# Performance work log

Hardware: AMD Instinct MI355X
Metric: run time of the kernel (lower is better)

## Reference

```python
import jax, jax.numpy as jnp
import numpy as np

B, N, D = 4, 2048, 1024
H = 16
HD = D // H          # 64
SCALE = 1.0 / HD     # module uses 1/head_dim (NOT 1/sqrt)
NEG = -10000.0       # masked_fill value used by the module
THETA = 10000.0


def setup_inputs() -> dict:
    key = jax.random.key(0)
    ks = jax.random.split(key, 6)
    s = (1.0 / D) ** 0.5  # init_method_normal((1/dim)**0.5)
    return {
        "x": jax.random.normal(ks[0], (B, N, D), jnp.float32),
        "Wq": jax.random.normal(ks[1], (D, D), jnp.float32) * s,
        "Wk": jax.random.normal(ks[2], (D, D), jnp.float32) * s,
        "Wv": jax.random.normal(ks[3], (D, D), jnp.float32) * s,
        "Wo": jax.random.normal(ks[4], (D, D), jnp.float32) * s,
        "bo": jnp.zeros((D,), jnp.float32),
    }


def _rope(t):
    # t: [b, h, n, d]; interleaved-pair rotary (lucidrains rotate_queries_or_keys)
    d, n = t.shape[-1], t.shape[-2]
    inv_freq = 1.0 / (THETA ** (jnp.arange(0, d, 2, dtype=jnp.float32) / d))  # [d/2]
    ang = jnp.arange(n, dtype=jnp.float32)[:, None] * inv_freq[None, :]        # [n, d/2]
    cos = jnp.repeat(jnp.cos(ang), 2, axis=-1)  # [n, d]
    sin = jnp.repeat(jnp.sin(ang), 2, axis=-1)
    x1, x2 = t[..., ::2], t[..., 1::2]
    rot = jnp.stack([-x2, x1], axis=-1).reshape(t.shape)  # rotate_half
    return t * cos + rot * sin


def reference(x, Wq, Wk, Wv, Wo, bo):
    b, n, _ = x.shape
    # QKV projections (no bias; torch Linear: x @ W.T)
    q = (x @ Wq.T).reshape(b, n, H, HD).transpose(0, 2, 1, 3)  # [b,h,n,d]
    k = (x @ Wk.T).reshape(b, n, H, HD).transpose(0, 2, 1, 3)
    v = (x @ Wv.T).reshape(b, n, H, HD).transpose(0, 2, 1, 3)
    # RoPE on q, k
    q = _rope(q)
    k = _rope(k)
    # additive mask: 0 on/below diagonal, -10000 above (causal_mask=True path)
    i = jnp.arange(n)
    add_mask = jnp.where(i[:, None] >= i[None, :], 0.0, NEG).astype(x.dtype)  # [n,n]
    scores = jnp.einsum("bhqd,bhkd->bhqk", q, k) * SCALE + add_mask
    attn = jax.nn.softmax(scores, axis=-1)
    out = jnp.einsum("bhqk,bhkd->bhqd", attn, v)            # [b,h,n,d]
    out = out.transpose(0, 2, 1, 3).reshape(b, n, H * HD)    # [b,n,D]
    return out @ Wo.T + bo
```

## Files before the change

### kernel.cpp

```cpp
#include <hip/hip_runtime.h>
#include <hip/hip_bf16.h>
#include <math.h>

#define B_ 4
#define N_ 2048
#define D_ 1024
#define H_ 16
#define HD_ 64
#define SCALE_ 0.015625f
#define MD_ ((size_t)B_ * N_ * D_)
#define DD_ ((size_t)D_ * D_)
#define BHSZ_ ((size_t)N_ * HD_)
#define QSC_ 0.0225421143f

typedef __hip_bfloat16 bf16;
typedef __attribute__((ext_vector_type(8))) __bf16 bf16x8;
typedef __attribute__((ext_vector_type(4))) float f32x4;
typedef __attribute__((ext_vector_type(16))) float f32x16;

__device__ __forceinline__ float b2f(bf16 x) { return __bfloat162float(x); }
__device__ __forceinline__ bf16 f2b(float x) { return __float2bfloat16(x); }

__device__ __forceinline__ unsigned int pk2(float a, float b) {
  union { bf16 h[2]; unsigned int u; } t;
  t.h[0] = f2b(a); t.h[1] = f2b(b);
  return t.u;
}
__device__ __forceinline__ unsigned int pk2t(float a, float b) {
  return (__float_as_uint(a) >> 16) | (__float_as_uint(b) & 0xffff0000u);
}

__device__ __forceinline__ void gl_lds16(const bf16* g, bf16* l) {
  __builtin_amdgcn_global_load_lds(
      (const __attribute__((address_space(1))) void*)g,
      (__attribute__((address_space(3))) void*)l, 16, 0, 0);
}

__global__ __launch_bounds__(256) void cvt_all(
    const float* __restrict__ x,  const float* __restrict__ wq,
    const float* __restrict__ wk, const float* __restrict__ wv,
    const float* __restrict__ wo, bf16* __restrict__ xb,
    bf16* __restrict__ wb)
{
  const int blk = blockIdx.x;
  const float* s; bf16* d; int i;
  if (blk < 4096)      { s = x;  d = xb;           i = blk; }
  else if (blk < 4608) { s = wq; d = wb;           i = blk - 4096; }
  else if (blk < 5120) { s = wk; d = wb + DD_;     i = blk - 4608; }
  else if (blk < 5632) { s = wv; d = wb + 2 * DD_; i = blk - 5120; }
  else                 { s = wo; d = wb + 3 * DD_; i = blk - 5632; }
  int e = (i * 256 + threadIdx.x) * 8;
  float4 a = *reinterpret_cast<const float4*>(s + e);
  float4 b = *reinterpret_cast<const float4*>(s + e + 4);
  bf16 t[8] = {f2b(a.x), f2b(a.y), f2b(a.z), f2b(a.w),
               f2b(b.x), f2b(b.y), f2b(b.z), f2b(b.w)};
  *reinterpret_cast<int4*>(d + e) = *reinterpret_cast<const int4*>(t);
}

template <int MODE>
__global__ __launch_bounds__(256) void mgemm(
    const bf16* __restrict__ A, const bf16* __restrict__ W,
    const float* __restrict__ bias, void* __restrict__ Cv,
    int M, int N, int K)
{
  __shared__ bf16 As[128 * 32];
  __shared__ bf16 Ws[128 * 32];

  const int tid  = threadIdx.x;
  const int w    = tid >> 6;
  const int lane = tid & 63;
  const int bm   = blockIdx.y * 128;
  const int bn   = blockIdx.x * 128;

  const int wr = (w >> 1) * 64;
  const int wc = (w & 1) * 64;
  const int lm   = lane & 15;
  const int quad = lane >> 4;

  const int srow = lane >> 2;
  const int sslot = (lane & 3) ^ ((lane >> 3) & 3);
  const int scol = sslot * 8;

  const int rsw  = (quad ^ ((lm >> 1) & 3)) * 8;

  f32x4 acc[4][4] = {};

  for (int k0 = 0; k0 < K; k0 += 32) {
#pragma unroll
    for (int cc = 0; cc < 2; ++cc) {
      int c = w * 2 + cc;
      int r = c * 16 + srow;
      gl_lds16(A + (size_t)(bm + r) * K + k0 + scol, &As[c * 512]);
      gl_lds16(W + (size_t)(bn + r) * K + k0 + scol, &Ws[c * 512]);
    }
    __syncthreads();

    bf16x8 af[4], bf_[4];
#pragma unroll
    for (int mi = 0; mi < 4; ++mi)
      af[mi] = *reinterpret_cast<const bf16x8*>(&As[(wr + mi * 16 + lm) * 32 + rsw]);
#pragma unroll
    for (int ni = 0; ni < 4; ++ni)
      bf_[ni] = *reinterpret_cast<const bf16x8*>(&Ws[(wc + ni * 16 + lm) * 32 + rsw]);

#pragma unroll
    for (int mi = 0; mi < 4; ++mi)
#pragma unroll
      for (int ni = 0; ni < 4; ++ni)
        acc[mi][ni] = __builtin_amdgcn_mfma_f32_16x16x32_bf16(
            af[mi], bf_[ni], acc[mi][ni], 0, 0, 0);
    __syncthreads();
  }

#pragma unroll
  for (int mi = 0; mi < 4; ++mi) {
#pragma unroll
    for (int r = 0; r < 4; ++r) {
      int row = bm + wr + mi * 16 + quad * 4 + r;
#pragma unroll
      for (int ni = 0; ni < 4; ++ni) {
        int col = bn + wc + ni * 16 + lm;
        float v = acc[mi][ni][r];
        if (MODE == 1) {
          v += bias[col];
          reinterpret_cast<float*>(Cv)[(size_t)row * N + col] = v;
        } else {
          int reg = col >> 10;
          int cc  = col & 1023;
          int bb  = row >> 11;
          int n   = row & (N_ - 1);
          int hh  = cc >> 6;
          int dd  = cc & 63;
          if (reg < 2) {
            int t32 = n >> 5, m = n & 31;
            int s = dd >> 4, hb = (dd >> 3) & 1, j = dd & 7;
            reinterpret_cast<bf16*>(Cv)[(size_t)reg * MD_ +
                (size_t)(bb * H_ + hh) * BHSZ_ +
                (size_t)t32 * 2048 + s * 512 + hb * 256 + m * 8 + j] = f2b(v);
          } else {
            int t32 = n >> 5, kk = n & 31;
            int hf = kk >> 4, hb = (kk >> 3) & 1, j = kk & 7;
            reinterpret_cast<bf16*>(Cv)[2 * MD_ +
                (size_t)(bb * H_ + hh) * BHSZ_ +
                (size_t)t32 * 2048 + hf * 1024 + hb * 512 + dd * 8 + j] = f2b(v);
          }
        }
      }
    }
  }
}

__global__ __launch_bounds__(256) void rope_inplace(bf16* __restrict__ qf,
                                                    bf16* __restrict__ kf)
{
  const int half = blockIdx.x >> 12;
  const int blk  = blockIdx.x & 4095;
  bf16* base = half ? kf : qf;
  const float LN_THETA = 9.210340371976184f;

  size_t e = ((size_t)blk * 256 + threadIdx.x) * 8;
  int within = (int)(e & (BHSZ_ - 1));
  int t32 = within >> 11;
  int rem = within & 2047;
  int s  = rem >> 9;
  int hb = (rem >> 8) & 1;
  int m  = (rem >> 3) & 31;
  int n  = t32 * 32 + m;

  uint4 raw = *reinterpret_cast<const uint4*>(base + e);
  unsigned int pr[4] = {raw.x, raw.y, raw.z, raw.w};
  unsigned int outw[4];
#pragma unroll
  for (int p = 0; p < 4; ++p) {
    int i = s * 8 + hb * 4 + p;
    float inv = __expf(-((float)(2 * i) / (float)HD_) * LN_THETA);
    float ang = (float)n * inv;
    float sv, cv;
    sincosf(ang, &sv, &cv);
    float a = b2f(((bf16*)&pr[p])[0]);
    float c = b2f(((bf16*)&pr[p])[1]);
    float r0 = a * cv - c * sv;
    float r1 = c * cv + a * sv;
    if (half == 0) { r0 *= QSC_; r1 *= QSC_; }
    outw[p] = pk2(r0, r1);
  }
  uint4 o = {outw[0], outw[1], outw[2], outw[3]};
  *reinterpret_cast<uint4*>(base + e) = o;
}

__global__ __launch_bounds__(128) void fattn4_kernel(
    const bf16* __restrict__ Qf, const bf16* __restrict__ Kf,
    const bf16* __restrict__ Vf, bf16* __restrict__ O)
{
  __shared__ float Ls[32 * 64];
  __shared__ float Ll[64];

  const int wv   = threadIdx.x >> 6;
  const int lane = threadIdx.x & 63;
  const int blk  = blockIdx.x;
  const int xcd  = blk & 7;
  const int j    = blk >> 3;
  const int qt   = 63 - (j >> 3);
  const int bh   = xcd * 8 + (j & 7);
  const int b    = bh >> 4;
  const int h    = bh & 15;
  const int col  = lane & 31;
  const int hi   = lane >> 5;

  const bf16* Qb = Qf + (size_t)bh * BHSZ_ + (size_t)qt * 2048 + hi * 256 + col * 8;
  const bf16* Kb = Kf + (size_t)bh * BHSZ_ + hi * 256 + col * 8;
  const bf16* Vb = Vf + (size_t)bh * BHSZ_ + hi * 512 + col * 8;

  bf16x8 qb[4];
#pragma unroll
  for (int s = 0; s < 4; ++s)
    qb[s] = *reinterpret_cast<const bf16x8*>(Qb + s * 512);

  f32x16 o0 = {}, o1 = {};
  float lsum = 0.f;

  for (int kst = wv; kst <= qt; kst += 2) {
    const bf16* kp = Kb + (size_t)kst * 2048;
    f32x16 st = {};
#pragma unroll
    for (int s = 0; s < 4; ++s) {
      bf16x8 ka = *reinterpret_cast<const bf16x8*>(kp + s * 512);
      st = __builtin_amdgcn_mfma_f32_32x32x16_bf16(ka, qb[s], st, 0, 0, 0);
    }

    float pe[16];
    if (kst == qt) {
#pragma unroll
      for (int r = 0; r < 16; ++r) {
        int koff = (r & 3) + 8 * (r >> 2) + 4 * hi;
        float e = (koff <= col) ? exp2f(st[r]) : 0.f;
        pe[r] = e; lsum += e;
      }
    } else {
#pragma unroll
      for (int r = 0; r < 16; ++r) {
        float e = exp2f(st[r]);
        pe[r] = e; lsum += e;
      }
    }

    const bf16* vp = Vb + (size_t)kst * 2048;
#pragma unroll
    for (int hf = 0; hf < 2; ++hf) {
      unsigned int a0 = pk2t(pe[8 * hf + 0], pe[8 * hf + 1]);
      unsigned int a1 = pk2t(pe[8 * hf + 2], pe[8 * hf + 3]);
      unsigned int b0 = pk2t(pe[8 * hf + 4], pe[8 * hf + 5]);
      unsigned int b1 = pk2t(pe[8 * hf + 6], pe[8 * hf + 7]);
      unsigned int s0 = hi ? a0 : b0;
      unsigned int s1 = hi ? a1 : b1;
      unsigned int r0 = (unsigned int)__shfl_xor((int)s0, 32);
      unsigned int r1 = (unsigned int)__shfl_xor((int)s1, 32);
      union { uint4 u; bf16x8 v; } pb;
      pb.u.x = hi ? r0 : a0;
      pb.u.y = hi ? r1 : a1;
      pb.u.z = hi ? b0 : r0;
      pb.u.w = hi ? b1 : r1;

      bf16x8 v0 = *reinterpret_cast<const bf16x8*>(vp + hf * 1024);
      bf16x8 v1 = *reinterpret_cast<const bf16x8*>(vp + hf * 1024 + 256);
      o0 = __builtin_amdgcn_mfma_f32_32x32x16_bf16(v0, pb.v, o0, 0, 0, 0);
      o1 = __builtin_amdgcn_mfma_f32_32x32x16_bf16(v1, pb.v, o1, 0, 0, 0);
    }
  }

  if (wv == 1) {
#pragma unroll
    for (int r = 0; r < 16; ++r) {
      Ls[r * 64 + lane]        = o0[r];
      Ls[(16 + r) * 64 + lane] = o1[r];
    }
    Ll[lane] = lsum;
  }
  __syncthreads();
  if (wv == 0) {
    float lt = lsum + Ll[lane];
    lt += __shfl_xor(lt, 32);
    float inv = 1.f / lt;
#pragma unroll
    for (int r = 0; r < 16; ++r) {
      o0[r] = (o0[r] + Ls[r * 64 + lane]) * inv;
      o1[r] = (o1[r] + Ls[(16 + r) * 64 + lane]) * inv;
    }
    bf16* Op = O + ((size_t)(b * N_ + 32 * qt + col)) * D_ + h * HD_;
#pragma unroll
    for (int g = 0; g < 4; ++g) {
      uint2 u;
      u.x = pk2(o0[4 * g + 0], o0[4 * g + 1]);
      u.y = pk2(o0[4 * g + 2], o0[4 * g + 3]);
      *reinterpret_cast<uint2*>(Op + 8 * g + 4 * hi) = u;
      u.x = pk2(o1[4 * g + 0], o1[4 * g + 1]);
      u.y = pk2(o1[4 * g + 2], o1[4 * g + 3]);
      *reinterpret_cast<uint2*>(Op + 32 + 8 * g + 4 * hi) = u;
    }
  }
}

extern "C" void kernel_launch(void* const* d_in, const int* in_sizes, int n_in,
                              void* d_out, int out_size, void* d_ws, size_t ws_size,
                              hipStream_t stream)
{
  const float* x  = (const float*)d_in[0];
  const float* Wq = (const float*)d_in[1];
  const float* Wk = (const float*)d_in[2];
  const float* Wv = (const float*)d_in[3];
  const float* Wo = (const float*)d_in[4];
  const float* bo = (const float*)d_in[5];
  float* out = (float*)d_out;

  const int M = B_ * N_;

  bf16* xb  = (bf16*)d_ws;
  bf16* qf  = xb + MD_;
  bf16* kf  = qf + MD_;
  bf16* vf  = kf + MD_;
  bf16* Wqb = vf + MD_;
  bf16* Wob = Wqb + 3 * DD_;
  bf16* ao  = xb;

  cvt_all<<<6144, 256, 0, stream>>>(x, Wq, Wk, Wv, Wo, xb, Wqb);

  mgemm<0><<<dim3(24, 64), 256, 0, stream>>>(xb, Wqb, nullptr, qf, M, 3 * D_, D_);

  rope_inplace<<<8192, 256, 0, stream>>>(qf, kf);

  fattn4_kernel<<<4096, 128, 0, stream>>>(qf, kf, vf, ao);

  mgemm<1><<<dim3(8, 64), 256, 0, stream>>>(ao, Wob, bo, out, M, D_, D_);
}
```

Before: 274.3 us.

## Give each attention wave its own query tile instead of splitting keys across waves

```diff
diff --git a/kernel.cpp b/kernel.cpp
--- a/kernel.cpp
+++ b/kernel.cpp
@@ -188,22 +188,20 @@
   *reinterpret_cast<uint4*>(base + e) = o;
 }
 
-__global__ __launch_bounds__(128) void fattn4_kernel(
+__global__ __launch_bounds__(128) void fattn5_kernel(
     const bf16* __restrict__ Qf, const bf16* __restrict__ Kf,
     const bf16* __restrict__ Vf, bf16* __restrict__ O)
 {
-  __shared__ float Ls[32 * 64];
-  __shared__ float Ll[64];
-
   const int wv   = threadIdx.x >> 6;
   const int lane = threadIdx.x & 63;
   const int blk  = blockIdx.x;
   const int xcd  = blk & 7;
-  const int j    = blk >> 3;
-  const int qt   = 63 - (j >> 3);
-  const int bh   = xcd * 8 + (j & 7);
+  const int jj   = blk >> 3;
+  const int j    = 31 - (jj >> 3);
+  const int bh   = xcd * 8 + (jj & 7);
   const int b    = bh >> 4;
   const int h    = bh & 15;
+  const int qt   = 2 * j + wv;
   const int col  = lane & 31;
   const int hi   = lane >> 5;
 
@@ -219,7 +217,7 @@
   f32x16 o0 = {}, o1 = {};
   float lsum = 0.f;
 
-  for (int kst = wv; kst <= qt; kst += 2) {
+  for (int kst = 0; kst <= qt; ++kst) {
     const bf16* kp = Kb + (size_t)kst * 2048;
     f32x16 st = {};
 #pragma unroll
@@ -268,35 +266,21 @@
     }
   }
 
-  if (wv == 1) {
-#pragma unroll
-    for (int r = 0; r < 16; ++r) {
-      Ls[r * 64 + lane]        = o0[r];
-      Ls[(16 + r) * 64 + lane] = o1[r];
-    }
-    Ll[lane] = lsum;
-  }
-  __syncthreads();
-  if (wv == 0) {
-    float lt = lsum + Ll[lane];
-    lt += __shfl_xor(lt, 32);
-    float inv = 1.f / lt;
-#pragma unroll
-    for (int r = 0; r < 16; ++r) {
-      o0[r] = (o0[r] + Ls[r * 64 + lane]) * inv;
-      o1[r] = (o1[r] + Ls[(16 + r) * 64 + lane]) * inv;
-    }
-    bf16* Op = O + ((size_t)(b * N_ + 32 * qt + col)) * D_ + h * HD_;
-#pragma unroll
-    for (int g = 0; g < 4; ++g) {
-      uint2 u;
-      u.x = pk2(o0[4 * g + 0], o0[4 * g + 1]);
-      u.y = pk2(o0[4 * g + 2], o0[4 * g + 3]);
-      *reinterpret_cast<uint2*>(Op + 8 * g + 4 * hi) = u;
-      u.x = pk2(o1[4 * g + 0], o1[4 * g + 1]);
-      u.y = pk2(o1[4 * g + 2], o1[4 * g + 3]);
-      *reinterpret_cast<uint2*>(Op + 32 + 8 * g + 4 * hi) = u;
-    }
+  float lt = lsum + __shfl_xor(lsum, 32);
+  float inv = 1.f / lt;
+#pragma unroll
+  for (int r = 0; r < 16; ++r) { o0[r] *= inv; o1[r] *= inv; }
+
+  bf16* Op = O + ((size_t)(b * N_ + 32 * qt + col)) * D_ + h * HD_;
+#pragma unroll
+  for (int g = 0; g < 4; ++g) {
+    uint2 u;
+    u.x = pk2(o0[4 * g + 0], o0[4 * g + 1]);
+    u.y = pk2(o0[4 * g + 2], o0[4 * g + 3]);
+    *reinterpret_cast<uint2*>(Op + 8 * g + 4 * hi) = u;
+    u.x = pk2(o1[4 * g + 0], o1[4 * g + 1]);
+    u.y = pk2(o1[4 * g + 2], o1[4 * g + 3]);
+    *reinterpret_cast<uint2*>(Op + 32 + 8 * g + 4 * hi) = u;
   }
 }
 
@@ -328,7 +312,7 @@
 
   rope_inplace<<<8192, 256, 0, stream>>>(qf, kf);
 
-  fattn4_kernel<<<4096, 128, 0, stream>>>(qf, kf, vf, ao);
+  fattn5_kernel<<<2048, 128, 0, stream>>>(qf, kf, vf, ao);
 
   mgemm<1><<<dim3(8, 64), 256, 0, stream>>>(ao, Wob, bo, out, M, D_, D_);
 }
```

New measurement: 331.4 us. 1.21x slower.
